# Kernel optimization log

Measured on AMD Instinct MI355X. Metric: run time of the kernel, lower is better.

The kernel has to match this reference:

```python
import jax, jax.numpy as jnp
import numpy as np

PARTITIONS = 8
TWO_PI = 2.0 * np.pi
EPS_COUNT = 0.0001  # added to bin counts to avoid div-by-zero


def setup_inputs() -> dict:
    key = jax.random.key(0)
    k1, k2, k3, k4 = jax.random.split(key, 4)
    B, N, T = 16384, 128, 8
    trajs = jax.random.normal(k1, (B, T, 2), dtype=jnp.float32)
    nei_trajs = jax.random.normal(k2, (B, N, T, 2), dtype=jnp.float32)
    # mark last 32 neighbors as invalid (all-zero trajectories -> masked out)
    nei_trajs = nei_trajs.at[:, N - 32:].set(0.0)
    # TrajEncoding: Dense(dim=3 -> output_units=128) + ReLU
    W_ce = jax.random.normal(k3, (3, 128), dtype=jnp.float32) * (1.0 / np.sqrt(3.0))
    b_ce = jnp.zeros((128,), dtype=jnp.float32)
    return {"trajs": trajs, "nei_trajs": nei_trajs, "W_ce": W_ce, "b_ce": b_ce}


def reference(trajs, nei_trajs, W_ce, b_ce):
    # trajs: [B, T, 2]; nei_trajs: [B, N, T, 2]
    nei_vector = nei_trajs[..., -1, :] - nei_trajs[..., 0, :]      # [B, N, 2]
    nei_pos = nei_trajs[..., -1, :]                                 # [B, N, 2]

    # factors (use_velocity, use_distance, use_direction; rel_velocity=False)
    f_velocity = jnp.linalg.norm(nei_vector, axis=-1)               # [B, N]
    f_distance = jnp.linalg.norm(nei_pos, axis=-1)                  # [B, N]
    f_direction = jnp.arctan2(nei_pos[..., 0], nei_pos[..., 1]) % TWO_PI  # [B, N]

    angle_idx = (f_direction / (TWO_PI / PARTITIONS)).astype(jnp.int32)   # [B, N]
    nei_mask = (jnp.sum(nei_trajs, axis=(-1, -2)) != 0).astype(jnp.int32)  # [B, N]
    angle_idx = angle_idx * nei_mask + (-1) * (1 - nei_mask)

    # one-hot over partitions replaces the python loop: [B, N, P]
    onehot = (angle_idx[..., None] == jnp.arange(PARTITIONS, dtype=jnp.int32)).astype(jnp.float32)
    n = jnp.sum(onehot, axis=1) + EPS_COUNT                         # [B, P]

    feats = jnp.stack([f_velocity, f_distance, f_direction], axis=-1)  # [B, N, 3]
    sums = jnp.einsum('bnf,bnp->bpf', feats, onehot)                # [B, P, 3]
    social_circle = sums / n[..., None]                             # [B, P, 3]

    f_sc = jax.nn.relu(social_circle @ W_ce + b_ce)                 # [B, P, 128]
    return f_sc, social_circle
```

## Files before the change

kernel.cpp:

```cpp
#include <hip/hip_runtime.h>
#include <math.h>

#define NPART 8
#define NN    128

typedef float f32x4 __attribute__((ext_vector_type(4)));

__global__ __launch_bounds__(256) void sc_kernel(
    const float* __restrict__ nei,
    const float* __restrict__ W,
    const float* __restrict__ bce,
    float* __restrict__ fsc,
    float* __restrict__ scout,
    int Btot)
{
    const int tid  = threadIdx.x;
    const int lane = tid & 63;
    const int wv   = tid >> 6;
    const int b    = blockIdx.x * 4 + wv;
    if (b >= Btot) return;

    __shared__ float s_sum[4][NPART * 3];
    __shared__ float s_cnt[4][NPART];
    __shared__ float s_sc[4][NPART * 3];

    const f32x4* src = reinterpret_cast<const f32x4*>(nei) + (size_t)b * (NN * 4);
    f32x4 a0 = __builtin_nontemporal_load(src + lane * 4 + 0);
    f32x4 c0 = __builtin_nontemporal_load(src + lane * 4 + 1);
    f32x4 d0 = __builtin_nontemporal_load(src + lane * 4 + 2);
    f32x4 e0 = __builtin_nontemporal_load(src + lane * 4 + 3);
    f32x4 a1 = __builtin_nontemporal_load(src + 256 + lane * 4 + 0);
    f32x4 c1 = __builtin_nontemporal_load(src + 256 + lane * 4 + 1);
    f32x4 d1 = __builtin_nontemporal_load(src + 256 + lane * 4 + 2);
    f32x4 e1 = __builtin_nontemporal_load(src + 256 + lane * 4 + 3);

    const int c0i = 4 * (lane & 31);
    f32x4 wr0 = *reinterpret_cast<const f32x4*>(W + 0 * NN + c0i);
    f32x4 wr1 = *reinterpret_cast<const f32x4*>(W + 1 * NN + c0i);
    f32x4 wr2 = *reinterpret_cast<const f32x4*>(W + 2 * NN + c0i);
    f32x4 bb  = *reinterpret_cast<const f32x4*>(bce + c0i);

    if (lane < NPART * 3) s_sum[wv][lane] = 0.0f;
    if (lane < NPART)     s_cnt[wv][lane] = 0.0f;
    __builtin_amdgcn_wave_barrier();

    const float TWOPI = 6.2831853071795864769f;
    const float STEP  = (float)(6.283185307179586 / 8.0);

    #pragma unroll
    for (int h = 0; h < 2; ++h) {
        f32x4 a = h ? a1 : a0;
        f32x4 c = h ? c1 : c0;
        f32x4 d = h ? d1 : d0;
        f32x4 e = h ? e1 : e0;

        float total = (((a.x + a.y) + (a.z + a.w)) + ((c.x + c.y) + (c.z + c.w)))
                    + (((d.x + d.y) + (d.z + d.w)) + ((e.x + e.y) + (e.z + e.w)));

        float px = e.z, py = e.w;
        float vx = px - a.x, vy = py - a.y;
        float fvel  = sqrtf(vx * vx + vy * vy);
        float fdist = sqrtf(px * px + py * py);

        float fdir = atan2f(px, py);
        if (fdir < 0.0f) fdir += TWOPI;

        int idx = (int)(fdir / STEP);

        if (total != 0.0f && idx >= 0 && idx < NPART) {
            atomicAdd(&s_sum[wv][idx * 3 + 0], fvel);
            atomicAdd(&s_sum[wv][idx * 3 + 1], fdist);
            atomicAdd(&s_sum[wv][idx * 3 + 2], fdir);
            atomicAdd(&s_cnt[wv][idx], 1.0f);
        }
    }
    __builtin_amdgcn_wave_barrier();

    if (lane < NPART * 3) {
        float v = s_sum[wv][lane] / (s_cnt[wv][lane / 3] + 0.0001f);
        s_sc[wv][lane] = v;
        __builtin_nontemporal_store(v, scout + (size_t)b * (NPART * 3) + lane);
    }
    __builtin_amdgcn_wave_barrier();

    float* o = fsc + (size_t)b * NPART * NN;
    #pragma unroll
    for (int s = 0; s < 4; ++s) {
        int p = 2 * s + (lane >> 5);
        float sv = s_sc[wv][p * 3 + 0];
        float sd = s_sc[wv][p * 3 + 1];
        float sr = s_sc[wv][p * 3 + 2];
        f32x4 acc;
        acc.x = fmaxf(fmaf(sv, wr0.x, fmaf(sd, wr1.x, fmaf(sr, wr2.x, bb.x))), 0.0f);
        acc.y = fmaxf(fmaf(sv, wr0.y, fmaf(sd, wr1.y, fmaf(sr, wr2.y, bb.y))), 0.0f);
        acc.z = fmaxf(fmaf(sv, wr0.z, fmaf(sd, wr1.z, fmaf(sr, wr2.z, bb.z))), 0.0f);
        acc.w = fmaxf(fmaf(sv, wr0.w, fmaf(sd, wr1.w, fmaf(sr, wr2.w, bb.w))), 0.0f);
        __builtin_nontemporal_store(acc, reinterpret_cast<f32x4*>(o + p * NN + c0i));
    }
}

extern "C" void kernel_launch(void* const* d_in, const int* in_sizes, int n_in,
                              void* d_out, int out_size, void* d_ws, size_t ws_size,
                              hipStream_t stream) {
    const float* nei = (const float*)d_in[1];
    const float* W   = (const float*)d_in[2];
    const float* bce = (const float*)d_in[3];

    const int Btot = in_sizes[1] / (NN * 8 * 2);

    float* fsc   = (float*)d_out;
    float* scout = fsc + (size_t)Btot * NPART * NN;

    const int nblk = (Btot + 3) / 4;
    sc_kernel<<<nblk, 256, 0, stream>>>(nei, W, bce, fsc, scout, Btot);
}
```

Measured before the change: 51.84 us.

## Split fused kernel into separate reduction and projection kernels

The single kernel that reduced neighbor features and then wrote the 8x128 projected output is split into two launches. The first computes the social circle and writes it to global memory. The second reads it back and computes the dense+ReLU projection for eight batch rows per block. Nontemporal loads and stores are also replaced with plain accesses. The split adds a launch and a round trip to global memory in exchange for simpler, more uniform streaming phases.

```diff
diff --git a/kernel.cpp b/kernel.cpp
--- a/kernel.cpp
+++ b/kernel.cpp
@@ -8,9 +8,6 @@
 
 __global__ __launch_bounds__(256) void sc_kernel(
     const float* __restrict__ nei,
-    const float* __restrict__ W,
-    const float* __restrict__ bce,
-    float* __restrict__ fsc,
     float* __restrict__ scout,
     int Btot)
 {
@@ -22,23 +19,16 @@
 
     __shared__ float s_sum[4][NPART * 3];
     __shared__ float s_cnt[4][NPART];
-    __shared__ float s_sc[4][NPART * 3];
 
     const f32x4* src = reinterpret_cast<const f32x4*>(nei) + (size_t)b * (NN * 4);
-    f32x4 a0 = __builtin_nontemporal_load(src + lane * 4 + 0);
-    f32x4 c0 = __builtin_nontemporal_load(src + lane * 4 + 1);
-    f32x4 d0 = __builtin_nontemporal_load(src + lane * 4 + 2);
-    f32x4 e0 = __builtin_nontemporal_load(src + lane * 4 + 3);
-    f32x4 a1 = __builtin_nontemporal_load(src + 256 + lane * 4 + 0);
-    f32x4 c1 = __builtin_nontemporal_load(src + 256 + lane * 4 + 1);
-    f32x4 d1 = __builtin_nontemporal_load(src + 256 + lane * 4 + 2);
-    f32x4 e1 = __builtin_nontemporal_load(src + 256 + lane * 4 + 3);
-
-    const int c0i = 4 * (lane & 31);
-    f32x4 wr0 = *reinterpret_cast<const f32x4*>(W + 0 * NN + c0i);
-    f32x4 wr1 = *reinterpret_cast<const f32x4*>(W + 1 * NN + c0i);
-    f32x4 wr2 = *reinterpret_cast<const f32x4*>(W + 2 * NN + c0i);
-    f32x4 bb  = *reinterpret_cast<const f32x4*>(bce + c0i);
+    f32x4 a0 = src[lane * 4 + 0];
+    f32x4 c0 = src[lane * 4 + 1];
+    f32x4 d0 = src[lane * 4 + 2];
+    f32x4 e0 = src[lane * 4 + 3];
+    f32x4 a1 = src[256 + lane * 4 + 0];
+    f32x4 c1 = src[256 + lane * 4 + 1];
+    f32x4 d1 = src[256 + lane * 4 + 2];
+    f32x4 e1 = src[256 + lane * 4 + 3];
 
     if (lane < NPART * 3) s_sum[wv][lane] = 0.0f;
     if (lane < NPART)     s_cnt[wv][lane] = 0.0f;
@@ -78,24 +68,51 @@
 
     if (lane < NPART * 3) {
         float v = s_sum[wv][lane] / (s_cnt[wv][lane / 3] + 0.0001f);
-        s_sc[wv][lane] = v;
-        __builtin_nontemporal_store(v, scout + (size_t)b * (NPART * 3) + lane);
+        scout[(size_t)b * (NPART * 3) + lane] = v;
     }
-    __builtin_amdgcn_wave_barrier();
+}
 
-    float* o = fsc + (size_t)b * NPART * NN;
+__global__ __launch_bounds__(256) void fsc_kernel(
+    const float* __restrict__ sc,
+    const float* __restrict__ W,
+    const float* __restrict__ bce,
+    float* __restrict__ fsc,
+    int Btot)
+{
+    const int tid = threadIdx.x;
+    const int p   = tid >> 5;
+    const int c0i = (tid & 31) * 4;
+
+    f32x4 wr0 = *reinterpret_cast<const f32x4*>(W + 0 * NN + c0i);
+    f32x4 wr1 = *reinterpret_cast<const f32x4*>(W + 1 * NN + c0i);
+    f32x4 wr2 = *reinterpret_cast<const f32x4*>(W + 2 * NN + c0i);
+    f32x4 bb  = *reinterpret_cast<const f32x4*>(bce + c0i);
+
+    const int base = blockIdx.x * 8;
+
+    float sv[8], sd[8], sr[8];
     #pragma unroll
-    for (int s = 0; s < 4; ++s) {
-        int p = 2 * s + (lane >> 5);
-        float sv = s_sc[wv][p * 3 + 0];
-        float sd = s_sc[wv][p * 3 + 1];
-        float sr = s_sc[wv][p * 3 + 2];
-        f32x4 acc;
-        acc.x = fmaxf(fmaf(sv, wr0.x, fmaf(sd, wr1.x, fmaf(sr, wr2.x, bb.x))), 0.0f);
-        acc.y = fmaxf(fmaf(sv, wr0.y, fmaf(sd, wr1.y, fmaf(sr, wr2.y, bb.y))), 0.0f);
-        acc.z = fmaxf(fmaf(sv, wr0.z, fmaf(sd, wr1.z, fmaf(sr, wr2.z, bb.z))), 0.0f);
-        acc.w = fmaxf(fmaf(sv, wr0.w, fmaf(sd, wr1.w, fmaf(sr, wr2.w, bb.w))), 0.0f);
-        __builtin_nontemporal_store(acc, reinterpret_cast<f32x4*>(o + p * NN + c0i));
+    for (int i = 0; i < 8; ++i) {
+        int b = base + i;
+        if (b < Btot) {
+            const float* s = sc + (size_t)b * (NPART * 3) + p * 3;
+            sv[i] = s[0];
+            sd[i] = s[1];
+            sr[i] = s[2];
+        }
+    }
+
+    #pragma unroll
+    for (int i = 0; i < 8; ++i) {
+        int b = base + i;
+        if (b < Btot) {
+            f32x4 acc;
+            acc.x = fmaxf(fmaf(sv[i], wr0.x, fmaf(sd[i], wr1.x, fmaf(sr[i], wr2.x, bb.x))), 0.0f);
+            acc.y = fmaxf(fmaf(sv[i], wr0.y, fmaf(sd[i], wr1.y, fmaf(sr[i], wr2.y, bb.y))), 0.0f);
+            acc.z = fmaxf(fmaf(sv[i], wr0.z, fmaf(sd[i], wr1.z, fmaf(sr[i], wr2.z, bb.z))), 0.0f);
+            acc.w = fmaxf(fmaf(sv[i], wr0.w, fmaf(sd[i], wr1.w, fmaf(sr[i], wr2.w, bb.w))), 0.0f);
+            *reinterpret_cast<f32x4*>(fsc + (size_t)b * NPART * NN + p * NN + c0i) = acc;
+        }
     }
 }
 
@@ -111,6 +128,6 @@
     float* fsc   = (float*)d_out;
     float* scout = fsc + (size_t)Btot * NPART * NN;
 
-    const int nblk = (Btot + 3) / 4;
-    sc_kernel<<<nblk, 256, 0, stream>>>(nei, W, bce, fsc, scout, Btot);
+    sc_kernel<<<(Btot + 3) / 4, 256, 0, stream>>>(nei, scout, Btot);
+    fsc_kernel<<<(Btot + 7) / 8, 256, 0, stream>>>(scout, W, bce, fsc, Btot);
 }
```

New measurement: 54.18 us. 4.5% more time.
